# Performance work log

Measured on AMD Instinct MI355X. Metric: run time of the kernel, lower is better.

Reference implementation:

```python
import jax, jax.numpy as jnp
import numpy as np

B, D_IN, T = 16, 1024, 4096
CB_SIZE, CB_DIM = 8192, 512
EPS = 1e-12


def _conv1d_s2(x, w):
    # x: [b, c_in, t], w: [c_out, c_in, 3]; stride 2, padding 1 (matches nn.Conv1d)
    return jax.lax.conv_general_dilated(
        x, w, window_strides=(2,), padding=[(1, 1)],
        dimension_numbers=("NCH", "OIH", "NCH"))


def _l2_normalize(v):
    # F.normalize(v, dim=1) semantics
    return v / jnp.maximum(jnp.linalg.norm(v, axis=1, keepdims=True), EPS)


def setup_inputs() -> dict:
    key = jax.random.key(0)
    k1, k2, k3, k4 = jax.random.split(key, 4)
    x = jax.random.normal(k1, (B, D_IN, T), dtype=jnp.float32)
    w1 = jax.random.normal(k2, (CB_DIM, D_IN, 3), dtype=jnp.float32) * 0.02
    w2 = jax.random.normal(k3, (CB_DIM, CB_DIM, 3), dtype=jnp.float32) * 0.02
    codebook = jax.random.normal(k4, (CB_SIZE, CB_DIM), dtype=jnp.float32)
    return {"x": x, "w1": w1, "w2": w2, "codebook": codebook}


def reference(x, w1, w2, codebook):
    # in_proj: two stride-2 convs -> [b, cb_dim, t], t = T // 4
    x_e = _conv1d_s2(_conv1d_s2(x, w1), w2)
    b, d, t = x_e.shape
    enc = x_e.transpose(0, 2, 1).reshape(b * t, d)   # (b t) d
    enc = _l2_normalize(enc)
    cb = _l2_normalize(codebook)
    # squared euclidean distance via matmul
    dist = (jnp.sum(enc * enc, axis=1, keepdims=True)
            - 2.0 * enc @ cb.T
            + jnp.sum(cb * cb, axis=1)[None, :])     # (b t) codebook_size
    indices = jnp.argmax(-dist, axis=1).reshape(b, t)
    return indices
```

## Files before the change

kernel.cpp:

```cpp
#include <hip/hip_runtime.h>


typedef __attribute__((ext_vector_type(8))) _Float16 f16x8;
typedef __attribute__((ext_vector_type(8))) short bf16x8;
typedef __attribute__((ext_vector_type(4))) float f32x4;

__device__ inline ushort f2bf(float x) {
  union { float f; unsigned u; } v; v.f = x;
  unsigned r = v.u + 0x7fffu + ((v.u >> 16) & 1u);
  return (ushort)(r >> 16);
}

__device__ inline void splitf(float v, ushort& h, ushort& l) {
  union { _Float16 h; ushort u; } a, b;
  a.h = (_Float16)v;
  b.h = (_Float16)(v - (float)a.h);
  h = a.u; l = b.u;
}

__global__ __launch_bounds__(256) void prep_w(const float* __restrict__ w,
                                              ushort* __restrict__ ws,
                                              int n ) {
  const int idx = blockIdx.x * 256 + threadIdx.x;
  if (idx >= n) return;
  const float v0 = w[(size_t)idx * 3 + 0];
  const float v1 = w[(size_t)idx * 3 + 1];
  const float v2 = w[(size_t)idx * 3 + 2];
  ushort h, l;
  splitf(v0, h, l); ws[idx] = h; ws[(size_t)n + idx] = l;
  splitf(v1, h, l); ws[2 * (size_t)n + idx] = h; ws[3 * (size_t)n + idx] = l;
  splitf(v2, h, l); ws[4 * (size_t)n + idx] = h; ws[5 * (size_t)n + idx] = l;
}

__global__ __launch_bounds__(256) void zero_halo(ushort* __restrict__ xo1,
                                                 ushort* __restrict__ xo2) {
  const int b = blockIdx.x, tid = threadIdx.x;
  const uint4 z = make_uint4(0, 0, 0, 0);
  *(uint4*)(xo1 + (size_t)b * 2049 * 2048 + tid * 8) = z;
  if (tid < 128) *(uint4*)(xo2 + (size_t)b * 1025 * 1024 + tid * 8) = z;
}

template <int CI, int T>
__global__ __launch_bounds__(256) void prep_x(const float* __restrict__ x,
                                              ushort* __restrict__ xe,
                                              ushort* __restrict__ xo) {
  const int t0 = blockIdx.x * 256;
  const int ci0 = blockIdx.y * 32;
  const int b = blockIdx.z;
  const int tid = threadIdx.x;
  __shared__ float tile[32][257];
  const int wv = tid >> 6, lane = tid & 63;
  const float* xb = x + ((size_t)b * CI + ci0) * T + t0;
#pragma unroll
  for (int r = 0; r < 8; r++) {
    const int ci = r * 4 + wv;
    const float4 v = *(const float4*)(xb + (size_t)ci * T + lane * 4);
    tile[ci][lane * 4 + 0] = v.x; tile[ci][lane * 4 + 1] = v.y;
    tile[ci][lane * 4 + 2] = v.z; tile[ci][lane * 4 + 3] = v.w;
  }
  __syncthreads();
  const int jj = tid >> 1, ph = tid & 1;
  const int tl = 2 * jj + ph;
  __attribute__((aligned(16))) ushort h[32], l[32];
#pragma unroll
  for (int c = 0; c < 32; c++) splitf(tile[c][tl], h[c], l[c]);
  constexpr int TH = T / 2;
  constexpr int RW = CI * 2;
  ushort* dst;
  if (ph == 0) dst = xe + ((size_t)b * TH + (t0 >> 1) + jj) * RW;
  else dst = xo + ((size_t)b * (TH + 1) + (t0 >> 1) + jj + 1) * RW;
  dst += (ci0 >> 5) * 64;
#pragma unroll
  for (int k = 0; k < 4; k++) {
    *(uint4*)(dst + k * 8) = *(const uint4*)(h + k * 8);
    *(uint4*)(dst + 32 + k * 8) = *(const uint4*)(l + k * 8);
  }
}

template <int C_IN, int T_OUT, bool SPLIT_OUT>
__global__ __launch_bounds__(256, 4) void conv_mfma(
    const ushort* __restrict__ xe, const ushort* __restrict__ xo,
    const ushort* __restrict__ ws, float* __restrict__ out,
    ushort* __restrict__ ye, ushort* __restrict__ yo) {
  const int co0 = blockIdx.x * 128;
  const int t0 = blockIdx.y * 64;
  const int b = blockIdx.z;
  const int tid = threadIdx.x;
  const int wv = tid >> 6, lane = tid & 63;
  const int l15 = lane & 15, quad = lane >> 4;

  __shared__ ushort xeh[64 * 40], xel[64 * 40], xoh[65 * 40], xol[65 * 40];

  f32x4 acc[2][4] = {};
  const int RW = C_IN * 2;
  const ushort* xe_b = xe + ((size_t)b * T_OUT + t0) * RW;
  const ushort* xo_b = xo + ((size_t)b * (T_OUT + 1) + t0) * RW;

  for (int ci0 = 0; ci0 < C_IN; ci0 += 32) {
    __syncthreads();
    const int choff = (ci0 >> 5) * 64;
#pragma unroll
    for (int q = 0; q < 5; q++) {
      const int id = tid + 256 * q;
      if (id < 1032) {
        const int g = id & 3;
        const int u = id >> 2;
        const uint4* src;
        ushort* dst;
        if (u < 128) {
          const int row = u >> 1, part = u & 1;
          src = (const uint4*)(xe_b + (size_t)row * RW + choff + part * 32 + g * 8);
          dst = (part ? xel : xeh) + row * 40 + g * 8;
        } else {
          const int u2 = u - 128;
          const int row = u2 >> 1, part = u2 & 1;
          src = (const uint4*)(xo_b + (size_t)row * RW + choff + part * 32 + g * 8);
          dst = (part ? xol : xoh) + row * 40 + g * 8;
        }
        *(uint4*)dst = *src;
      }
    }
    __syncthreads();

#pragma unroll
    for (int koff = 0; koff < 3; koff++) {
      f16x8 a_h[2], a_l[2];
#pragma unroll
      for (int i = 0; i < 2; i++) {
        const size_t co = (size_t)co0 + wv * 32 + i * 16 + l15;
        const ushort* wp = ws + ((size_t)(koff * 2) * 512) * C_IN + co * C_IN + ci0 + quad * 8;
        a_h[i] = *(const f16x8*)wp;
        a_l[i] = *(const f16x8*)(wp + (size_t)512 * C_IN);
      }
      const ushort* bh = (koff == 1) ? xeh : xoh;
      const ushort* bl = (koff == 1) ? xel : xol;
      const int radd = (koff == 2) ? 1 : 0;
#pragma unroll
      for (int j = 0; j < 4; j++) {
        const int row = j * 16 + l15 + radd;
        const f16x8 b_h = *(const f16x8*)(bh + row * 40 + quad * 8);
        const f16x8 b_l = *(const f16x8*)(bl + row * 40 + quad * 8);
#pragma unroll
        for (int i = 0; i < 2; i++) {
          acc[i][j] = __builtin_amdgcn_mfma_f32_16x16x32_f16(a_h[i], b_h, acc[i][j], 0, 0, 0);
          acc[i][j] = __builtin_amdgcn_mfma_f32_16x16x32_f16(a_h[i], b_l, acc[i][j], 0, 0, 0);
          acc[i][j] = __builtin_amdgcn_mfma_f32_16x16x32_f16(a_l[i], b_h, acc[i][j], 0, 0, 0);
        }
      }
    }
  }

  if (SPLIT_OUT) {
#pragma unroll
    for (int i = 0; i < 2; i++) {
      const int ch = (co0 >> 5) + wv;
      const int ci32 = i * 16 + quad * 4;
#pragma unroll
      for (int j = 0; j < 4; j++) {
        const int t = t0 + j * 16 + l15;
        const int ph = t & 1;
        const int row = (t >> 1) + ph;
        __attribute__((aligned(8))) ushort h[4], l[4];
#pragma unroll
        for (int r = 0; r < 4; r++) splitf(acc[i][j][r], h[r], l[r]);
        ushort* dst = (ph ? yo : ye) +
                      ((size_t)b * (ph ? 1025 : 1024) + row) * 1024 + ch * 64 + ci32;
        *(uint2*)dst = *(const uint2*)h;
        *(uint2*)(dst + 32) = *(const uint2*)l;
      }
    }
  } else {
#pragma unroll
    for (int i = 0; i < 2; i++) {
#pragma unroll
      for (int j = 0; j < 4; j++) {
        const int t = t0 + j * 16 + l15;
        const int co = co0 + wv * 32 + i * 16 + quad * 4;
        const float4 v = make_float4(acc[i][j][0], acc[i][j][1], acc[i][j][2], acc[i][j][3]);
        *(float4*)(out + ((size_t)b * T_OUT + t) * 512 + co) = v;
      }
    }
  }
}

__global__ __launch_bounds__(64) void norm_rows(const float* __restrict__ out2t,
                                                float* __restrict__ enc,
                                                ushort* __restrict__ enc16) {
  const int row = blockIdx.x;
  const int lane = threadIdx.x;
  const float* p = out2t + (size_t)row * 512 + lane * 8;
  const float4 v0 = *(const float4*)p;
  const float4 v1 = *(const float4*)(p + 4);
  float ss = v0.x * v0.x + v0.y * v0.y + v0.z * v0.z + v0.w * v0.w +
             v1.x * v1.x + v1.y * v1.y + v1.z * v1.z + v1.w * v1.w;
#pragma unroll
  for (int m = 32; m >= 1; m >>= 1) ss += __shfl_xor(ss, m, 64);
  const float inv = 1.0f / fmaxf(sqrtf(ss), 1e-12f);
  float4 a, c;
  a.x = v0.x * inv; a.y = v0.y * inv; a.z = v0.z * inv; a.w = v0.w * inv;
  c.x = v1.x * inv; c.y = v1.y * inv; c.z = v1.z * inv; c.w = v1.w * inv;
  float* eo = enc + (size_t)row * 512 + lane * 8;
  *(float4*)eo = a;
  *(float4*)(eo + 4) = c;
  __attribute__((aligned(16))) ushort u[8] = {
      f2bf(a.x), f2bf(a.y), f2bf(a.z), f2bf(a.w),
      f2bf(c.x), f2bf(c.y), f2bf(c.z), f2bf(c.w)};
  *(uint4*)(enc16 + (size_t)row * 512 + lane * 8) = *(const uint4*)u;
}

__global__ __launch_bounds__(256) void norm_cb(const float* __restrict__ cb,
                                               float* __restrict__ cbn,
                                               ushort* __restrict__ cbn16,
                                               float* __restrict__ cb2) {
  const int row = blockIdx.x * 4 + (threadIdx.x >> 6);
  const int lane = threadIdx.x & 63;
  const float* p = cb + (long)row * 512;
  const float4 v0 = *(const float4*)(p + lane * 4);
  const float4 v1 = *(const float4*)(p + 256 + lane * 4);
  float ss = v0.x * v0.x + v0.y * v0.y + v0.z * v0.z + v0.w * v0.w +
             v1.x * v1.x + v1.y * v1.y + v1.z * v1.z + v1.w * v1.w;
#pragma unroll
  for (int m = 32; m >= 1; m >>= 1) ss += __shfl_xor(ss, m, 64);
  const float n = fmaxf(sqrtf(ss), 1e-12f);
  float4 a, c;
  a.x = v0.x / n; a.y = v0.y / n; a.z = v0.z / n; a.w = v0.w / n;
  c.x = v1.x / n; c.y = v1.y / n; c.z = v1.z / n; c.w = v1.w / n;
  *(float4*)(cbn + (long)row * 512 + lane * 4) = a;
  *(float4*)(cbn + (long)row * 512 + 256 + lane * 4) = c;
  ushort4 ua, uc;
  ua.x = f2bf(a.x); ua.y = f2bf(a.y); ua.z = f2bf(a.z); ua.w = f2bf(a.w);
  uc.x = f2bf(c.x); uc.y = f2bf(c.y); uc.z = f2bf(c.z); uc.w = f2bf(c.w);
  *(ushort4*)(cbn16 + (long)row * 512 + lane * 4) = ua;
  *(ushort4*)(cbn16 + (long)row * 512 + 256 + lane * 4) = uc;
  float s2 = a.x * a.x + a.y * a.y + a.z * a.z + a.w * a.w +
             c.x * c.x + c.y * c.y + c.z * c.z + c.w * c.w;
#pragma unroll
  for (int m = 32; m >= 1; m >>= 1) s2 += __shfl_xor(s2, m, 64);
  if (lane == 0) cb2[row] = s2;
}

__device__ inline void top2_merge(float& s1, int& i1, float& s2, int& i2,
                                  float t1, int j1, float t2, int j2) {
  if (t1 > s1) {
    if (s1 > t2) { s2 = s1; i2 = i1; } else { s2 = t2; i2 = j2; }
    s1 = t1; i1 = j1;
  } else if (t1 > s2) {
    s2 = t1; i2 = j1;
  }
}

__global__ __launch_bounds__(256, 3) void score_top2(
    const ushort* __restrict__ enc16, const ushort* __restrict__ cbn16,
    const float* __restrict__ cb2, float* __restrict__ pscore,
    int* __restrict__ pidx) {
  const int nt = blockIdx.x;
  const int mt = blockIdx.y;
  const int m0 = mt * 128, n0 = nt * 128;
  const int tid = threadIdx.x;
  const int wave = tid >> 6, lane = tid & 63;
  const int wm = wave & 1, wn = wave >> 1;
  const int quad = lane >> 4, l15 = lane & 15;

  f32x4 acc[4][4] = {};

  const ushort* arow = enc16 + ((size_t)(m0 + wm * 64 + l15) * 512) + quad * 8;
  const ushort* brow = cbn16 + ((size_t)(n0 + wn * 64 + l15) * 512) + quad * 8;

  for (int k0 = 0; k0 < 512; k0 += 64) {
#pragma unroll
    for (int kk = 0; kk < 2; kk++) {
      const int k = k0 + kk * 32;
      bf16x8 af[4], bf[4];
#pragma unroll
      for (int i = 0; i < 4; i++)
        af[i] = *(const bf16x8*)(arow + (size_t)(i * 16) * 512 + k);
#pragma unroll
      for (int j = 0; j < 4; j++)
        bf[j] = *(const bf16x8*)(brow + (size_t)(j * 16) * 512 + k);
#pragma unroll
      for (int i = 0; i < 4; i++)
#pragma unroll
        for (int j = 0; j < 4; j++)
          acc[i][j] = __builtin_amdgcn_mfma_f32_16x16x32_bf16(af[i], bf[j], acc[i][j], 0, 0, 0);
    }
  }

  float cb2c[4];
  int coln[4];
#pragma unroll
  for (int j = 0; j < 4; j++) {
    coln[j] = n0 + wn * 64 + j * 16 + l15;
    cb2c[j] = cb2[coln[j]];
  }

#pragma unroll
  for (int mi = 0; mi < 4; mi++) {
#pragma unroll
    for (int i = 0; i < 4; i++) {
      float s1 = -3.4e38f, s2 = -3.4e38f;
      int i1 = -1, i2 = -1;
#pragma unroll
      for (int j = 0; j < 4; j++) {
        const float s = 2.0f * acc[mi][j][i] - cb2c[j];
        if (s > s1) { s2 = s1; i2 = i1; s1 = s; i1 = coln[j]; }
        else if (s > s2) { s2 = s; i2 = coln[j]; }
      }
#pragma unroll
      for (int m = 8; m >= 1; m >>= 1) {
        const float t1 = __shfl_xor(s1, m, 64);
        const int j1 = __shfl_xor(i1, m, 64);
        const float t2 = __shfl_xor(s2, m, 64);
        const int j2 = __shfl_xor(i2, m, 64);
        top2_merge(s1, i1, s2, i2, t1, j1, t2, j2);
      }
      if (l15 == 0) {
        const int row_g = m0 + wm * 64 + mi * 16 + quad * 4 + i;
        const size_t base = (size_t)row_g * 256 + (size_t)nt * 4 + wn * 2;
        pscore[base] = s1; pidx[base] = i1;
        pscore[base + 1] = s2; pidx[base + 1] = i2;
      }
    }
  }
}

__global__ __launch_bounds__(256) void rescore_argmax(
    const float* __restrict__ enc, const float* __restrict__ cbn,
    const float* __restrict__ cb2, const float* __restrict__ pscore,
    const int* __restrict__ pidx, int* __restrict__ out) {
  const int row = blockIdx.x;
  const int tid = threadIdx.x;
  __shared__ float wbest[4];
  __shared__ int wslot[4];
  __shared__ int winner;
  __shared__ int cand[8];
  __shared__ float fsc[8];
  __shared__ int fid[8];

  float s = pscore[(size_t)row * 256 + tid];
  const int id = pidx[(size_t)row * 256 + tid];

  for (int it = 0; it < 8; it++) {
    float bs = s;
    int bslot = tid;
#pragma unroll
    for (int m = 32; m >= 1; m >>= 1) {
      const float os = __shfl_xor(bs, m, 64);
      const int oslot = __shfl_xor(bslot, m, 64);
      if (os > bs || (os == bs && oslot < bslot)) { bs = os; bslot = oslot; }
    }
    if ((tid & 63) == 0) { wbest[tid >> 6] = bs; wslot[tid >> 6] = bslot; }
    __syncthreads();
    if (tid == 0) {
      float b = wbest[0]; int sl = wslot[0];
      for (int wv = 1; wv < 4; wv++)
        if (wbest[wv] > b || (wbest[wv] == b && wslot[wv] < sl)) { b = wbest[wv]; sl = wslot[wv]; }
      winner = sl;
    }
    __syncthreads();
    if (tid == winner) { cand[it] = id; s = -3.4e38f; }
    __syncthreads();
  }

  const int c = cand[tid >> 5];
  const float* ep = enc + (size_t)row * 512;
  const float* cp = cbn + (size_t)c * 512;
  float dot = 0.0f;
  const int d0 = (tid & 31) * 16;
#pragma unroll
  for (int u = 0; u < 4; u++) {
    const float4 e4 = *(const float4*)(ep + d0 + u * 4);
    const float4 c4 = *(const float4*)(cp + d0 + u * 4);
    dot = fmaf(e4.x, c4.x, dot);
    dot = fmaf(e4.y, c4.y, dot);
    dot = fmaf(e4.z, c4.z, dot);
    dot = fmaf(e4.w, c4.w, dot);
  }
#pragma unroll
  for (int m = 16; m >= 1; m >>= 1) dot += __shfl_xor(dot, m, 64);
  if ((tid & 31) == 0) {
    fsc[tid >> 5] = 2.0f * dot - cb2[c];
    fid[tid >> 5] = c;
  }
  __syncthreads();
  if (tid == 0) {
    float b = fsc[0]; int bi = fid[0];
    for (int q = 1; q < 8; q++)
      if (fsc[q] > b || (fsc[q] == b && fid[q] < bi)) { b = fsc[q]; bi = fid[q]; }
    out[row] = bi;
  }
}

extern "C" void kernel_launch(void* const* d_in, const int* in_sizes, int n_in,
                              void* d_out, int out_size, void* d_ws, size_t ws_size,
                              hipStream_t stream) {
  const float* x = (const float*)d_in[0];
  const float* w1 = (const float*)d_in[1];
  const float* w2 = (const float*)d_in[2];
  const float* cb = (const float*)d_in[3];
  int* out = (int*)d_out;

  char* w0 = (char*)d_ws;
  const size_t MB = 1ull << 20;
  ushort* xe1 = (ushort*)(w0);
  ushort* xo1 = (ushort*)(w0 + 128 * MB);
  ushort* xe2 = (ushort*)(w0 + 257 * MB);
  ushort* xo2 = (ushort*)(w0 + 289 * MB);
  ushort* ws1 = (ushort*)(w0 + 322 * MB);
  ushort* ws2 = (ushort*)(w0 + 328 * MB);
  float* out2t = (float*)(w0);
  float* enc = (float*)(w0 + 32 * MB);
  ushort* enc16 = (ushort*)(w0 + 64 * MB);
  float* cbn = (float*)(w0 + 80 * MB);
  ushort* cbn16 = (ushort*)(w0 + 96 * MB);
  float* cb2 = (float*)(w0 + 104 * MB);
  float* pscore = (float*)(w0 + 112 * MB);
  int* pidx = (int*)(w0 + 128 * MB);

  zero_halo<<<16, 256, 0, stream>>>(xo1, xo2);
  prep_w<<<2048, 256, 0, stream>>>(w1, ws1, 512 * 1024);
  prep_w<<<1024, 256, 0, stream>>>(w2, ws2, 512 * 512);
  prep_x<1024, 4096><<<dim3(16, 32, 16), 256, 0, stream>>>(x, xe1, xo1);
  conv_mfma<1024, 2048, true><<<dim3(4, 32, 16), 256, 0, stream>>>(
      xe1, xo1, ws1, nullptr, xe2, xo2);
  conv_mfma<512, 1024, false><<<dim3(4, 16, 16), 256, 0, stream>>>(
      xe2, xo2, ws2, out2t, nullptr, nullptr);
  norm_rows<<<16384, 64, 0, stream>>>(out2t, enc, enc16);
  norm_cb<<<2048, 256, 0, stream>>>(cb, cbn, cbn16, cb2);
  score_top2<<<dim3(64, 128), 256, 0, stream>>>(enc16, cbn16, cb2, pscore, pidx);
  rescore_argmax<<<16384, 256, 0, stream>>>(enc, cbn, cb2, pscore, pidx, out);
}
```

Before: 1.975 ms.

## Stage codebook stripe in swizzled LDS and stream encoder rows per wave

The score kernel now loads a 64-column codebook stripe (64x512 bf16, 64KB) into XOR-swizzled shared memory once per block. Eight waves then each stream 64-row encoder tiles directly from global memory across 2048 rows. Codebook operands come from LDS instead of repeated global loads, which cuts global traffic for B. The trade-off is 64KB of LDS per block, which limits occupancy. Each wave's A tile is still read from global without reuse across waves, and the grid shrinks to 1024 blocks of 512 threads.

```diff
diff --git a/kernel.cpp b/kernel.cpp
--- a/kernel.cpp
+++ b/kernel.cpp
@@ -249,75 +249,80 @@
   }
 }
 
-__global__ __launch_bounds__(256, 3) void score_top2(
+__global__ __launch_bounds__(512, 4) void score_top2(
     const ushort* __restrict__ enc16, const ushort* __restrict__ cbn16,
     const float* __restrict__ cb2, float* __restrict__ pscore,
     int* __restrict__ pidx) {
-  const int nt = blockIdx.x;
-  const int mt = blockIdx.y;
-  const int m0 = mt * 128, n0 = nt * 128;
+  const int mg = blockIdx.x;
+  const int stripe = blockIdx.y;
+  const int n0 = stripe * 64;
   const int tid = threadIdx.x;
   const int wave = tid >> 6, lane = tid & 63;
-  const int wm = wave & 1, wn = wave >> 1;
   const int quad = lane >> 4, l15 = lane & 15;
 
-  f32x4 acc[4][4] = {};
-
-  const ushort* arow = enc16 + ((size_t)(m0 + wm * 64 + l15) * 512) + quad * 8;
-  const ushort* brow = cbn16 + ((size_t)(n0 + wn * 64 + l15) * 512) + quad * 8;
-
-  for (int k0 = 0; k0 < 512; k0 += 64) {
-#pragma unroll
-    for (int kk = 0; kk < 2; kk++) {
-      const int k = k0 + kk * 32;
+  __shared__ __attribute__((aligned(16))) ushort blds[64 * 512];
+
+  for (int idx = tid; idx < 4096; idx += 512) {
+    const int col = idx >> 6, g = idx & 63;
+    const uint4 v = *(const uint4*)(cbn16 + (size_t)(n0 + col) * 512 + g * 8);
+    *(uint4*)(blds + col * 512 + ((g ^ (col & 7)) * 8)) = v;
+  }
+  __syncthreads();
+
+  float cb2c[4];
+#pragma unroll
+  for (int j = 0; j < 4; j++) cb2c[j] = cb2[n0 + j * 16 + l15];
+
+  for (int t = 0; t < 4; t++) {
+    const int m0 = mg * 2048 + (t * 8 + wave) * 64;
+    const ushort* arow = enc16 + (size_t)(m0 + l15) * 512 + quad * 8;
+
+    f32x4 acc[4][4] = {};
+#pragma unroll 2
+    for (int k0 = 0; k0 < 512; k0 += 32) {
+      const int gk = (k0 >> 3) + quad;
       bf16x8 af[4], bf[4];
 #pragma unroll
       for (int i = 0; i < 4; i++)
-        af[i] = *(const bf16x8*)(arow + (size_t)(i * 16) * 512 + k);
-#pragma unroll
-      for (int j = 0; j < 4; j++)
-        bf[j] = *(const bf16x8*)(brow + (size_t)(j * 16) * 512 + k);
+        af[i] = *(const bf16x8*)(arow + (size_t)(i * 16) * 512 + k0);
+#pragma unroll
+      for (int j = 0; j < 4; j++) {
+        const int col = j * 16 + l15;
+        bf[j] = *(const bf16x8*)(blds + col * 512 + ((gk ^ (col & 7)) * 8));
+      }
 #pragma unroll
       for (int i = 0; i < 4; i++)
 #pragma unroll
         for (int j = 0; j < 4; j++)
           acc[i][j] = __builtin_amdgcn_mfma_f32_16x16x32_bf16(af[i], bf[j], acc[i][j], 0, 0, 0);
     }
-  }
-
-  float cb2c[4];
-  int coln[4];
-#pragma unroll
-  for (int j = 0; j < 4; j++) {
-    coln[j] = n0 + wn * 64 + j * 16 + l15;
-    cb2c[j] = cb2[coln[j]];
-  }
-
-#pragma unroll
-  for (int mi = 0; mi < 4; mi++) {
-#pragma unroll
-    for (int i = 0; i < 4; i++) {
-      float s1 = -3.4e38f, s2 = -3.4e38f;
-      int i1 = -1, i2 = -1;
-#pragma unroll
-      for (int j = 0; j < 4; j++) {
-        const float s = 2.0f * acc[mi][j][i] - cb2c[j];
-        if (s > s1) { s2 = s1; i2 = i1; s1 = s; i1 = coln[j]; }
-        else if (s > s2) { s2 = s; i2 = coln[j]; }
-      }
-#pragma unroll
-      for (int m = 8; m >= 1; m >>= 1) {
-        const float t1 = __shfl_xor(s1, m, 64);
-        const int j1 = __shfl_xor(i1, m, 64);
-        const float t2 = __shfl_xor(s2, m, 64);
-        const int j2 = __shfl_xor(i2, m, 64);
-        top2_merge(s1, i1, s2, i2, t1, j1, t2, j2);
-      }
-      if (l15 == 0) {
-        const int row_g = m0 + wm * 64 + mi * 16 + quad * 4 + i;
-        const size_t base = (size_t)row_g * 256 + (size_t)nt * 4 + wn * 2;
-        pscore[base] = s1; pidx[base] = i1;
-        pscore[base + 1] = s2; pidx[base + 1] = i2;
+
+#pragma unroll
+    for (int mi = 0; mi < 4; mi++) {
+#pragma unroll
+      for (int i = 0; i < 4; i++) {
+        float s1 = -3.4e38f, s2 = -3.4e38f;
+        int i1 = -1, i2 = -1;
+#pragma unroll
+        for (int j = 0; j < 4; j++) {
+          const float s = 2.0f * acc[mi][j][i] - cb2c[j];
+          if (s > s1) { s2 = s1; i2 = i1; s1 = s; i1 = n0 + j * 16 + l15; }
+          else if (s > s2) { s2 = s; i2 = n0 + j * 16 + l15; }
+        }
+#pragma unroll
+        for (int m = 8; m >= 1; m >>= 1) {
+          const float t1 = __shfl_xor(s1, m, 64);
+          const int j1 = __shfl_xor(i1, m, 64);
+          const float t2 = __shfl_xor(s2, m, 64);
+          const int j2 = __shfl_xor(i2, m, 64);
+          top2_merge(s1, i1, s2, i2, t1, j1, t2, j2);
+        }
+        if (l15 == 0) {
+          const int row_g = m0 + mi * 16 + quad * 4 + i;
+          const size_t base = (size_t)row_g * 256 + (size_t)stripe * 2;
+          pscore[base] = s1; pidx[base] = i1;
+          pscore[base + 1] = s2; pidx[base + 1] = i2;
+        }
       }
     }
   }
@@ -426,6 +431,6 @@
       xe2, xo2, ws2, out2t, nullptr, nullptr);
   norm_rows<<<16384, 64, 0, stream>>>(out2t, enc, enc16);
   norm_cb<<<2048, 256, 0, stream>>>(cb, cbn, cbn16, cb2);
-  score_top2<<<dim3(64, 128), 256, 0, stream>>>(enc16, cbn16, cb2, pscore, pidx);
+  score_top2<<<dim3(8, 128), 512, 0, stream>>>(enc16, cbn16, cb2, pscore, pidx);
   rescore_argmax<<<16384, 256, 0, stream>>>(enc, cbn, cb2, pscore, pidx, out);
 }
```

Measured after the change: 1.752 ms. 11.3% less time.
